# Kernel tuning notes

Measured on AMD Instinct MI355X. Metric: run time of the kernel, lower is better.

The kernel has to match this reference:

```python
import jax, jax.numpy as jnp
import numpy as np

C = 256   # in_channels
H = 48
W = 48
B = 2     # batch after chunking into 3 frames; input batch = 3*B
F = 3     # frames (torch.chunk(x, 3))
G = 4     # GroupNorm groups
EPS = 1e-6


def setup_inputs() -> dict:
    key = jax.random.key(0)
    ks = jax.random.split(key, 10)
    s = C ** -0.5  # keep q/k magnitudes sane so softmax is not saturated
    return {
        "x":    jax.random.normal(ks[0], (F * B, C, H, W), jnp.float32),
        "gn_w": jnp.ones((C,), jnp.float32),
        "gn_b": jnp.zeros((C,), jnp.float32),
        "wq":   jax.random.normal(ks[1], (C, C), jnp.float32) * s,
        "bq":   jax.random.normal(ks[2], (C,), jnp.float32) * 0.02,
        "wk":   jax.random.normal(ks[3], (C, C), jnp.float32) * s,
        "bk":   jax.random.normal(ks[4], (C,), jnp.float32) * 0.02,
        "wv":   jax.random.normal(ks[5], (C, C), jnp.float32) * s,
        "bv":   jax.random.normal(ks[6], (C,), jnp.float32) * 0.02,
        "wp":   jax.random.normal(ks[7], (C, C), jnp.float32) * s,
        "bp":   jax.random.normal(ks[8], (C,), jnp.float32) * 0.02,
    }


def reference(x, gn_w, gn_b, wq, bq, wk, bk, wv, bv, wp, bp):
    B3, c, h, w = x.shape
    b = B3 // F
    # torch.chunk(x, 3) + stack(dim=2) -> (b, c, f, h, w); chunk index is frame
    hx = jnp.moveaxis(x.reshape(F, b, c, h, w), 0, 2)  # (b, c, f, h, w)

    # GroupNorm(num_groups=4, eps=1e-6, affine)
    hg = hx.reshape(b, G, c // G, F, h, w)
    mu = hg.mean(axis=(2, 3, 4, 5), keepdims=True)
    var = hg.var(axis=(2, 3, 4, 5), keepdims=True)
    hn = ((hg - mu) * jax.lax.rsqrt(var + EPS)).reshape(b, c, F, h, w)
    hn = hn * gn_w[None, :, None, None, None] + gn_b[None, :, None, None, None]

    # 1x1x1 Conv3d == channel matmul over flattened tokens n = (f h w)
    n = F * h * w
    hf = hn.reshape(b, c, n)                                  # (b, c, n)
    q = jnp.einsum('oc,bcn->bon', wq, hf) + bq[None, :, None]
    k = jnp.einsum('oc,bcn->bon', wk, hf) + bk[None, :, None]
    v = jnp.einsum('oc,bcn->bon', wv, hf) + bv[None, :, None]

    # scores[b,n,m] = sum_c q[b,c,n] * k[b,c,m], scaled by c^-0.5, softmax over m
    scores = jnp.einsum('bcn,bcm->bnm', q, k) * (c ** -0.5)
    attn = jax.nn.softmax(scores, axis=-1)                    # (b, n, n)

    # out[b,c,n] = sum_m v[b,c,m] * attn[b,n,m]
    o = jnp.einsum('bcm,bnm->bcn', v, attn)
    o = jnp.einsum('oc,bcn->bon', wp, o) + bp[None, :, None]  # proj_out

    o = o.reshape(b, c, F, h, w)
    # permute(0,2,1,3,4) then merge (b f) -> batch (b-major, f-minor)
    o = jnp.moveaxis(o, 2, 1).reshape(B3, c, h, w)
    return x + o
```

## Files before the change

kernel.cpp:

```cpp
#include <hip/hip_runtime.h>
#include <stdint.h>

#define CDIM 256
#define HW 2304
#define FR 3
#define NBATCH 2
#define NTOK 6912
#define EPSV 1e-6f
#define QSCALE (0.0625f * 1.44269504088896f)

typedef __attribute__((ext_vector_type(8))) short short8;
typedef __attribute__((ext_vector_type(4))) short short4v;
typedef __attribute__((ext_vector_type(4))) float f32x4;
typedef __attribute__((ext_vector_type(16))) float f32x16;
typedef __attribute__((ext_vector_type(4))) uint32_t u32x4;
typedef unsigned short u16;

__device__ inline u16 f2bf(float f) {
  union { float f; uint32_t u; } v; v.f = f;
  uint32_t r = v.u + 0x7FFFu + ((v.u >> 16) & 1u);
  return (u16)(r >> 16);
}
__device__ inline float bf2f(u16 h) {
  union { uint32_t u; float f; } v; v.u = ((uint32_t)h) << 16; return v.f;
}
__device__ inline void gload16(const void* g, void* l) {
  __builtin_amdgcn_global_load_lds(
      (const __attribute__((address_space(1))) void*)g,
      (__attribute__((address_space(3))) void*)l, 16, 0, 0);
}

__global__ void pre_k(const float* x, float* part, const float* wq,
                      const float* wk, const float* wv, const float* wp,
                      u16* wb) {
  if (blockIdx.x >= 256) {
    int idx = (blockIdx.x - 256) * 256 + threadIdx.x;
    wb[0 * 65536 + idx] = f2bf(wq[idx] * QSCALE);
    wb[1 * 65536 + idx] = f2bf(wk[idx]);
    wb[2 * 65536 + idx] = f2bf(wv[idx]);
    wb[3 * 65536 + idx] = f2bf(wp[idx]);
    return;
  }
  int bg = blockIdx.x >> 5, sl = blockIdx.x & 31;
  int b = bg >> 2, g = bg & 3;
  int tid = threadIdx.x;
  float s1 = 0.f, s2 = 0.f;
  for (int i = tid; i < 2 * NTOK; i += 256) {
    int cl = sl * 2 + (i / NTOK); int rem = i % NTOK;
    int f = rem / HW; int hw = rem - f * HW;
    float v = x[((size_t)(f * NBATCH + b) * CDIM + g * 64 + cl) * HW + hw];
    s1 += v; s2 += v * v;
  }
  #pragma unroll
  for (int m = 32; m >= 1; m >>= 1) {
    s1 += __shfl_xor(s1, m, 64);
    s2 += __shfl_xor(s2, m, 64);
  }
  __shared__ float r1[4], r2[4];
  int wid = tid >> 6;
  if ((tid & 63) == 0) { r1[wid] = s1; r2[wid] = s2; }
  __syncthreads();
  if (tid == 0) {
    part[blockIdx.x * 2 + 0] = r1[0] + r1[1] + r1[2] + r1[3];
    part[blockIdx.x * 2 + 1] = r2[0] + r2[1] + r2[2] + r2[3];
  }
}

__global__ void gn_fin_k(const float* part, float* stats) {
  int tid = threadIdx.x;
  if (tid < 8) {
    float s1 = 0.f, s2 = 0.f;
    for (int s = 0; s < 32; ++s) {
      s1 += part[(tid * 32 + s) * 2 + 0];
      s2 += part[(tid * 32 + s) * 2 + 1];
    }
    float inv = 1.f / (64.f * NTOK);
    float mu = s1 * inv;
    float var = s2 * inv - mu * mu;
    stats[tid * 2 + 0] = mu;
    stats[tid * 2 + 1] = rsqrtf(var + EPSV);
  }
}

__global__ void gn_apply_k(const float* x, const float* gn_w, const float* gn_b,
                           const float* stats, u16* hn) {
  int nt = blockIdx.x, ct = blockIdx.y, b = blockIdx.z;
  int tid = threadIdx.x;
  __shared__ float tile[64][65];
  int n0 = nt * 64; int f = n0 / HW; int hw0 = n0 - f * HW;
  float mu = stats[(b * 4 + ct) * 2 + 0];
  float rs = stats[(b * 4 + ct) * 2 + 1];
  #pragma unroll
  for (int i = 0; i < 16; ++i) {
    int lin = i * 256 + tid;
    int cr = lin >> 6, nc = lin & 63;
    int c = ct * 64 + cr;
    float v = x[((size_t)(f * NBATCH + b) * CDIM + c) * HW + hw0 + nc];
    tile[cr][nc] = (v - mu) * rs * gn_w[c] + gn_b[c];
  }
  __syncthreads();
  #pragma unroll
  for (int i = 0; i < 16; ++i) {
    int lin = i * 256 + tid;
    int nr = lin >> 6, cc = lin & 63;
    hn[((size_t)b * NTOK + n0 + nr) * CDIM + ct * 64 + cc] = f2bf(tile[cc][nr]);
  }
}

__global__ __launch_bounds__(256) void qkv_k(const u16* hn, const u16* wb,
    const float* bq, const float* bk, const float* bv,
    u16* qb, u16* kb, u16* vb) {
  int nt = blockIdx.x;
  int op = blockIdx.y >> 1, b = blockIdx.y & 1;
  int tid = threadIdx.x, lane = tid & 63, wid = tid >> 6;
  int lr = lane & 15, lg = lane >> 4;
  __shared__ __align__(16) char hn_lds[32768];
  {
    const char* src = (const char*)(hn + ((size_t)b * NTOK + nt * 64) * CDIM);
    #pragma unroll
    for (int i = 0; i < 8; ++i) {
      int off = i * 4096 + wid * 1024 + lane * 16;
      int row = off >> 9;
      gload16(src + (off ^ ((row & 7) << 4)), hn_lds + i * 4096 + wid * 1024);
    }
  }
  __syncthreads();
  f32x4 acc[16];
  #pragma unroll
  for (int i = 0; i < 16; ++i) acc[i] = (f32x4){0.f, 0.f, 0.f, 0.f};
  const u16* wsrc = wb + op * 65536;
  __builtin_amdgcn_s_setprio(1);
  #pragma unroll
  for (int cc = 0; cc < 4; ++cc) {
    short8 afr[2];
    #pragma unroll
    for (int kc = 0; kc < 2; ++kc) {
      int row = wid * 16 + lr;
      int byte = row * 512 + (cc * 64 + kc * 32 + lg * 8) * 2;
      afr[kc] = *(const short8*)(hn_lds + (byte ^ ((row & 7) << 4)));
    }
    #pragma unroll
    for (int cot = 0; cot < 16; ++cot) {
      #pragma unroll
      for (int kc = 0; kc < 2; ++kc) {
        short8 bfr = *(const short8*)(wsrc + (size_t)(cot * 16 + lr) * CDIM +
                                      cc * 64 + kc * 32 + lg * 8);
        if (op == 2)
          acc[cot] = __builtin_amdgcn_mfma_f32_16x16x32_bf16(afr[kc], bfr, acc[cot], 0, 0, 0);
        else
          acc[cot] = __builtin_amdgcn_mfma_f32_16x16x32_bf16(bfr, afr[kc], acc[cot], 0, 0, 0);
      }
    }
  }
  __builtin_amdgcn_s_setprio(0);
  if (op == 2) {
    int m0 = wid * 16 + lg * 4;
    char* vtile = (char*)vb + (size_t)b * NTOK * CDIM * 2 + (size_t)nt * 32768;
    int mchunk = (m0 >> 3);
    #pragma unroll
    for (int cot = 0; cot < 16; ++cot) {
      int co = cot * 16 + lr;
      float bb = bv[co];
      short4v r;
      #pragma unroll
      for (int j = 0; j < 4; ++j) r[j] = (short)f2bf(acc[cot][j] + bb);
      *(short4v*)(vtile + mchunk * 4096 + co * 16 + (lg & 1) * 8) = r;
    }
  } else {
    int row = wid * 16 + lr;
    int n = nt * 64 + row;
    const float* bias = (op == 0) ? bq : bk;
    float bscale = (op == 0) ? QSCALE : 1.0f;
    char* ktile = (char*)kb + (size_t)b * NTOK * CDIM * 2 + (size_t)nt * 32768;
    #pragma unroll
    for (int cot = 0; cot < 16; ++cot) {
      int co = cot * 16 + lg * 4;
      f32x4 b4 = *(const f32x4*)(bias + co);
      short4v r;
      #pragma unroll
      for (int j = 0; j < 4; ++j) r[j] = (short)f2bf(acc[cot][j] + b4[j] * bscale);
      if (op == 0) {
        *(short4v*)(qb + ((size_t)b * NTOK + n) * CDIM + co) = r;
      } else {
        int colchunk = cot * 2 + (lg >> 1);
        *(short4v*)(ktile + colchunk * 1024 + row * 16 + (lg & 1) * 8) = r;
      }
    }
  }
}

template <bool SPLIT>
__global__ __launch_bounds__(512, 2) void flash_k(const u16* qb, const u16* kb,
                                                  const u16* vb, u16* opart,
                                                  float* ml, u16* ob) {
  int qt = blockIdx.x, b = blockIdx.y, sp = blockIdx.z;
  int tid = threadIdx.x, lane = tid & 63, wid = tid >> 6;
  int ln = lane & 31, hi = lane >> 5;
  __shared__ __align__(16) char k_lds[2][32768];
  __shared__ __align__(16) char v_lds[2][32768];

  int t0 = SPLIT ? 27 * sp : 0;
  int t1 = SPLIT ? 27 * sp + 27 : 108;

  int nq = qt * 256 + wid * 32 + ln;
  const u16* qsrc = qb + ((size_t)b * NTOK + nq) * CDIM;
  short8 qf[16];
  #pragma unroll
  for (int ks = 0; ks < 16; ++ks)
    qf[ks] = *(const short8*)(qsrc + ks * 16 + hi * 8);

  float mrun = -1e30f, lrun = 0.f;
  f32x16 o[8];
  #pragma unroll
  for (int i = 0; i < 8; ++i)
    #pragma unroll
    for (int j = 0; j < 16; ++j) o[i][j] = 0.f;

  const char* kbb = (const char*)(kb + (size_t)b * NTOK * CDIM);
  const char* vbb = (const char*)(vb + (size_t)b * NTOK * CDIM);
  int kbase = hi * 1024 + ln * 16;
  int vbase = hi * 4096 + ln * 16;

  {
    const char* ks_ = kbb + (size_t)t0 * 32768;
    const char* vs_ = vbb + (size_t)t0 * 32768;
    #pragma unroll
    for (int i = 0; i < 8; ++i) {
      int ch = i * 8 + wid;
      if (ch < 32) gload16(ks_ + ch * 1024 + lane * 16, k_lds[0] + ch * 1024);
      else gload16(vs_ + (ch - 32) * 1024 + lane * 16, v_lds[0] + (ch - 32) * 1024);
    }
  }
  __syncthreads();

  for (int t = t0; t < t1; ++t) {
    int cur = (t - t0) & 1;
    if (t + 1 < t1) {
      const char* ks_ = kbb + (size_t)(t + 1) * 32768;
      const char* vs_ = vbb + (size_t)(t + 1) * 32768;
      #pragma unroll
      for (int i = 0; i < 8; ++i) {
        int ch = i * 8 + wid;
        if (ch < 32) gload16(ks_ + ch * 1024 + lane * 16, k_lds[cur ^ 1] + ch * 1024);
        else gload16(vs_ + (ch - 32) * 1024 + lane * 16, v_lds[cur ^ 1] + (ch - 32) * 1024);
      }
    }
    const char* kc = k_lds[cur] + kbase;
    const char* vc = v_lds[cur] + vbase;

    #pragma unroll
    for (int mt = 0; mt < 2; ++mt) {
      f32x16 S;
      #pragma unroll
      for (int j = 0; j < 16; ++j) S[j] = 0.f;
      __builtin_amdgcn_s_setprio(1);
      #pragma unroll
      for (int ks = 0; ks < 16; ++ks) {
        short8 kf = *(const short8*)(kc + ks * 2048 + mt * 512);
        S = __builtin_amdgcn_mfma_f32_32x32x16_bf16(kf, qf[ks], S, 0, 0, 0);
      }
      __builtin_amdgcn_s_setprio(0);
      float px = S[0];
      #pragma unroll
      for (int j = 1; j < 16; ++j) px = fmaxf(px, S[j]);
      px = fmaxf(px, __shfl_xor(px, 32, 64));
      if (__any(px > mrun + 10.0f)) {
        float mn = fmaxf(mrun, px);
        float r = exp2f(mrun - mn);
        mrun = mn; lrun *= r;
        #pragma unroll
        for (int i = 0; i < 8; ++i)
          #pragma unroll
          for (int j = 0; j < 16; ++j) o[i][j] *= r;
      }
      float lsum = 0.f;
      #pragma unroll
      for (int j = 0; j < 16; ++j) {
        float p = exp2f(S[j] - mrun);
        S[j] = p; lsum += p;
      }
      lsum += __shfl_xor(lsum, 32, 64);
      lrun += lsum;
      #pragma unroll
      for (int lks = 0; lks < 2; ++lks) {
        int rb = lks * 8;
        uint32_t x0, x1, y0, y1;
        asm("v_cvt_pk_bf16_f32 %0, %1, %2" : "=v"(x0) : "v"(S[rb + 0]), "v"(S[rb + 1]));
        asm("v_cvt_pk_bf16_f32 %0, %1, %2" : "=v"(x1) : "v"(S[rb + 2]), "v"(S[rb + 3]));
        asm("v_cvt_pk_bf16_f32 %0, %1, %2" : "=v"(y0) : "v"(S[rb + 4]), "v"(S[rb + 5]));
        asm("v_cvt_pk_bf16_f32 %0, %1, %2" : "=v"(y1) : "v"(S[rb + 6]), "v"(S[rb + 7]));
        asm("v_permlane32_swap_b32 %0, %1" : "+v"(x0), "+v"(y0));
        asm("v_permlane32_swap_b32 %0, %1" : "+v"(x1), "+v"(y1));
        u32x4 pd = (u32x4){x0, x1, y0, y1};
        short8 pf = *(short8*)&pd;
        __builtin_amdgcn_s_setprio(1);
        #pragma unroll
        for (int ct = 0; ct < 8; ++ct) {
          short8 vf = *(const short8*)(vc + (mt * 2 + lks) * 8192 + ct * 512);
          o[ct] = __builtin_amdgcn_mfma_f32_32x32x16_bf16(vf, pf, o[ct], 0, 0, 0);
        }
        __builtin_amdgcn_s_setprio(0);
      }
    }
    __syncthreads();
  }

  if (!SPLIT) {
    float linv = 1.0f / lrun;
    u16* d0 = ob + ((size_t)b * NTOK + nq) * CDIM;
    #pragma unroll
    for (int ct = 0; ct < 8; ++ct) {
      #pragma unroll
      for (int rq = 0; rq < 4; ++rq) {
        short4v r4;
        #pragma unroll
        for (int j = 0; j < 4; ++j) r4[j] = (short)f2bf(o[ct][rq * 4 + j] * linv);
        *(short4v*)(d0 + ct * 32 + rq * 8 + hi * 4) = r4;
      }
    }
  } else {
    u16* d0 = opart + ((size_t)(sp * 2 + b) * NTOK + nq) * CDIM;
    #pragma unroll
    for (int ct = 0; ct < 8; ++ct) {
      #pragma unroll
      for (int rq = 0; rq < 4; ++rq) {
        short4v r4;
        #pragma unroll
        for (int j = 0; j < 4; ++j) r4[j] = (short)f2bf(o[ct][rq * 4 + j]);
        *(short4v*)(d0 + ct * 32 + rq * 8 + hi * 4) = r4;
      }
    }
    if (hi == 0) {
      size_t mb = (size_t)(sp * 2 + b) * 2;
      ml[(mb + 0) * NTOK + nq] = mrun;
      ml[(mb + 1) * NTOK + nq] = lrun;
    }
  }
}

template <bool SPLIT>
__global__ __launch_bounds__(256) void proj_k(const u16* ob, const u16* opart,
    const float* ml, const u16* wb, const float* bp, const float* x, float* out) {
  int nt = blockIdx.x, b = blockIdx.y;
  int tid = threadIdx.x, lane = tid & 63, wid = tid >> 6;
  int lr = lane & 15, lg = lane >> 4;
  __shared__ __align__(16) char o_lds[32768];
  const u16* wpb = wb + 3 * 65536;
  if (SPLIT) {
    #pragma unroll
    for (int i = 0; i < 8; ++i) {
      int off = i * 4096 + tid * 16;
      int row = off >> 9;
      int c0 = (off & 511) >> 1;
      int n = nt * 64 + row;
      float mm[4], llv[4];
      #pragma unroll
      for (int s = 0; s < 4; ++s) {
        mm[s] = ml[((size_t)(s * 2 + b) * 2 + 0) * NTOK + n];
        llv[s] = ml[((size_t)(s * 2 + b) * 2 + 1) * NTOK + n];
      }
      float M = fmaxf(fmaxf(mm[0], mm[1]), fmaxf(mm[2], mm[3]));
      float w[4]; float den = 0.f;
      #pragma unroll
      for (int s = 0; s < 4; ++s) { w[s] = exp2f(mm[s] - M); den += w[s] * llv[s]; }
      float inv = 1.f / den;
      float o[8] = {0.f, 0.f, 0.f, 0.f, 0.f, 0.f, 0.f, 0.f};
      #pragma unroll
      for (int s = 0; s < 4; ++s) {
        short8 v = *(const short8*)(opart + ((size_t)(s * 2 + b) * NTOK + n) * CDIM + c0);
        #pragma unroll
        for (int j = 0; j < 8; ++j) o[j] += w[s] * bf2f((u16)v[j]);
      }
      short8 r8;
      #pragma unroll
      for (int j = 0; j < 8; ++j) r8[j] = (short)f2bf(o[j] * inv);
      *(short8*)(o_lds + (off ^ ((row & 7) << 4))) = r8;
    }
  } else {
    const char* src = (const char*)(ob + ((size_t)b * NTOK + nt * 64) * CDIM);
    #pragma unroll
    for (int i = 0; i < 8; ++i) {
      int off = i * 4096 + wid * 1024 + lane * 16;
      int row = off >> 9;
      gload16(src + (off ^ ((row & 7) << 4)), o_lds + i * 4096 + wid * 1024);
    }
  }
  __syncthreads();
  #pragma unroll
  for (int ct2 = 0; ct2 < 4; ++ct2) {
    int cot = wid * 4 + ct2;
    short8 aw[8];
    #pragma unroll
    for (int kc = 0; kc < 8; ++kc)
      aw[kc] = *(const short8*)(wpb + (size_t)(cot * 16 + lr) * CDIM + kc * 32 + lg * 8);
    #pragma unroll
    for (int ntile = 0; ntile < 4; ++ntile) {
      f32x4 a = (f32x4){0.f, 0.f, 0.f, 0.f};
      #pragma unroll
      for (int kc = 0; kc < 8; ++kc) {
        int row = ntile * 16 + lr;
        int byte = row * 512 + (kc * 32 + lg * 8) * 2;
        short8 bfr = *(const short8*)(o_lds + (byte ^ ((row & 7) << 4)));
        a = __builtin_amdgcn_mfma_f32_16x16x32_bf16(aw[kc], bfr, a, 0, 0, 0);
      }
      int n = nt * 64 + ntile * 16 + lr;
      int f = n / HW; int hw = n - f * HW;
      #pragma unroll
      for (int j = 0; j < 4; ++j) {
        int co = cot * 16 + lg * 4 + j;
        float val = a[j] + bp[co];
        size_t oi = ((size_t)(b * FR + f) * CDIM + co) * HW + hw;
        out[oi] = x[oi] + val;
      }
    }
  }
}

extern "C" void kernel_launch(void* const* d_in, const int* in_sizes, int n_in,
                              void* d_out, int out_size, void* d_ws, size_t ws_size,
                              hipStream_t stream) {
  const float* x    = (const float*)d_in[0];
  const float* gn_w = (const float*)d_in[1];
  const float* gn_b = (const float*)d_in[2];
  const float* wq   = (const float*)d_in[3];
  const float* bq   = (const float*)d_in[4];
  const float* wk   = (const float*)d_in[5];
  const float* bk   = (const float*)d_in[6];
  const float* wv   = (const float*)d_in[7];
  const float* bv   = (const float*)d_in[8];
  const float* wp   = (const float*)d_in[9];
  const float* bp   = (const float*)d_in[10];
  float* out = (float*)d_out;
  char* ws = (char*)d_ws;

  float* stats = (float*)(ws + 0);
  float* part  = (float*)(ws + 256);
  u16* wb = (u16*)(ws + 4096);
  u16* hn = (u16*)(ws + 528384);
  u16* qb = (u16*)(ws + 7606272);
  u16* kb = (u16*)(ws + 14684160);
  u16* vb = (u16*)(ws + 21762048);
  u16* ob = (u16*)(ws + 28839936);
  u16* opart = (u16*)(ws + 35917824);
  float* ml  = (float*)(ws + 64229376);
  const size_t NEED_SPLIT = 64671744;

  pre_k<<<512, 256, 0, stream>>>(x, part, wq, wk, wv, wp, wb);
  gn_fin_k<<<1, 64, 0, stream>>>(part, stats);
  gn_apply_k<<<dim3(108, 4, 2), 256, 0, stream>>>(x, gn_w, gn_b, stats, hn);
  qkv_k<<<dim3(108, 6), 256, 0, stream>>>(hn, wb, bq, bk, bv, qb, kb, vb);
  if (ws_size >= NEED_SPLIT) {
    flash_k<true><<<dim3(27, 2, 4), 512, 0, stream>>>(qb, kb, vb, opart, ml, ob);
    proj_k<true><<<dim3(108, 2), 256, 0, stream>>>(ob, opart, ml, wb, bp, x, out);
  } else {
    flash_k<false><<<dim3(27, 2, 1), 512, 0, stream>>>(qb, kb, vb, opart, ml, ob);
    proj_k<false><<<dim3(108, 2), 256, 0, stream>>>(ob, opart, ml, wb, bp, x, out);
  }
}
```

Before: 216.3 us.

## Fuse GroupNorm finalize, apply and QKV projection into one kernel

Merges the GroupNorm stats finalization, normalization/transpose and QKV projection into a single kernel. Each block now reduces the partial sums itself, normalizes its 64-token tile straight into LDS as bf16, and loops over the three projections. This removes two kernel launches and the global round trip of the normalized activation buffer. In exchange the grid shrinks from 648 to 216 blocks, each doing three times the matmul work, which lowers parallelism on a many-CU device.

```diff
diff --git a/kernel.cpp b/kernel.cpp
--- a/kernel.cpp
+++ b/kernel.cpp
@@ -66,124 +66,125 @@
   }
 }
 
-__global__ void gn_fin_k(const float* part, float* stats) {
-  int tid = threadIdx.x;
-  if (tid < 8) {
-    float s1 = 0.f, s2 = 0.f;
-    for (int s = 0; s < 32; ++s) {
-      s1 += part[(tid * 32 + s) * 2 + 0];
-      s2 += part[(tid * 32 + s) * 2 + 1];
-    }
-    float inv = 1.f / (64.f * NTOK);
-    float mu = s1 * inv;
-    float var = s2 * inv - mu * mu;
-    stats[tid * 2 + 0] = mu;
-    stats[tid * 2 + 1] = rsqrtf(var + EPSV);
-  }
-}
-
-__global__ void gn_apply_k(const float* x, const float* gn_w, const float* gn_b,
-                           const float* stats, u16* hn) {
-  int nt = blockIdx.x, ct = blockIdx.y, b = blockIdx.z;
-  int tid = threadIdx.x;
-  __shared__ float tile[64][65];
-  int n0 = nt * 64; int f = n0 / HW; int hw0 = n0 - f * HW;
-  float mu = stats[(b * 4 + ct) * 2 + 0];
-  float rs = stats[(b * 4 + ct) * 2 + 1];
-  #pragma unroll
-  for (int i = 0; i < 16; ++i) {
-    int lin = i * 256 + tid;
-    int cr = lin >> 6, nc = lin & 63;
-    int c = ct * 64 + cr;
-    float v = x[((size_t)(f * NBATCH + b) * CDIM + c) * HW + hw0 + nc];
-    tile[cr][nc] = (v - mu) * rs * gn_w[c] + gn_b[c];
-  }
-  __syncthreads();
-  #pragma unroll
-  for (int i = 0; i < 16; ++i) {
-    int lin = i * 256 + tid;
-    int nr = lin >> 6, cc = lin & 63;
-    hn[((size_t)b * NTOK + n0 + nr) * CDIM + ct * 64 + cc] = f2bf(tile[cc][nr]);
-  }
-}
-
-__global__ __launch_bounds__(256) void qkv_k(const u16* hn, const u16* wb,
+__global__ __launch_bounds__(256) void qkvf_k(const float* x, const float* part,
+    const float* gn_w, const float* gn_b, const u16* wb,
     const float* bq, const float* bk, const float* bv,
     u16* qb, u16* kb, u16* vb) {
-  int nt = blockIdx.x;
-  int op = blockIdx.y >> 1, b = blockIdx.y & 1;
+  int nt = blockIdx.x, b = blockIdx.y;
   int tid = threadIdx.x, lane = tid & 63, wid = tid >> 6;
   int lr = lane & 15, lg = lane >> 4;
   __shared__ __align__(16) char hn_lds[32768];
-  {
-    const char* src = (const char*)(hn + ((size_t)b * NTOK + nt * 64) * CDIM);
+  __shared__ float tile[64][65];
+  __shared__ float sstat[8];
+
+  if (tid < 128) {
+    int g = (tid >> 5) & 3, s = tid & 31;
+    float p1 = part[((b * 4 + g) * 32 + s) * 2 + 0];
+    float p2 = part[((b * 4 + g) * 32 + s) * 2 + 1];
+    #pragma unroll
+    for (int m = 1; m < 32; m <<= 1) {
+      p1 += __shfl_xor(p1, m, 64);
+      p2 += __shfl_xor(p2, m, 64);
+    }
+    if (s == 0) {
+      float inv = 1.f / (64.f * NTOK);
+      float mu = p1 * inv;
+      float var = p2 * inv - mu * mu;
+      sstat[g * 2 + 0] = mu;
+      sstat[g * 2 + 1] = rsqrtf(var + EPSV);
+    }
+  }
+  __syncthreads();
+
+  int n0 = nt * 64; int f = n0 / HW; int hw0 = n0 - f * HW;
+  #pragma unroll
+  for (int ct = 0; ct < 4; ++ct) {
+    float mu = sstat[ct * 2 + 0];
+    float rs = sstat[ct * 2 + 1];
+    #pragma unroll
+    for (int i = 0; i < 16; ++i) {
+      int lin = i * 256 + tid;
+      int cr = lin >> 6, nc = lin & 63;
+      int c = ct * 64 + cr;
+      float v = x[((size_t)(f * NBATCH + b) * CDIM + c) * HW + hw0 + nc];
+      tile[cr][nc] = (v - mu) * rs * gn_w[c] + gn_b[c];
+    }
+    __syncthreads();
     #pragma unroll
     for (int i = 0; i < 8; ++i) {
-      int off = i * 4096 + wid * 1024 + lane * 16;
-      int row = off >> 9;
-      gload16(src + (off ^ ((row & 7) << 4)), hn_lds + i * 4096 + wid * 1024);
-    }
-  }
-  __syncthreads();
-  f32x4 acc[16];
-  #pragma unroll
-  for (int i = 0; i < 16; ++i) acc[i] = (f32x4){0.f, 0.f, 0.f, 0.f};
-  const u16* wsrc = wb + op * 65536;
-  __builtin_amdgcn_s_setprio(1);
-  #pragma unroll
-  for (int cc = 0; cc < 4; ++cc) {
-    short8 afr[2];
-    #pragma unroll
-    for (int kc = 0; kc < 2; ++kc) {
+      int lin = i * 256 + tid;
+      int nr = lin >> 5, cp = lin & 31;
+      int cc = cp * 2;
+      uint32_t pk = (uint32_t)f2bf(tile[cc][nr]) |
+                    ((uint32_t)f2bf(tile[cc + 1][nr]) << 16);
+      int byte = nr * 512 + (ct * 64 + cc) * 2;
+      *(uint32_t*)(hn_lds + (byte ^ ((nr & 7) << 4))) = pk;
+    }
+    __syncthreads();
+  }
+
+  #pragma unroll
+  for (int op = 0; op < 3; ++op) {
+    f32x4 acc[16];
+    #pragma unroll
+    for (int i = 0; i < 16; ++i) acc[i] = (f32x4){0.f, 0.f, 0.f, 0.f};
+    const u16* wsrc = wb + op * 65536;
+    __builtin_amdgcn_s_setprio(1);
+    #pragma unroll
+    for (int cc = 0; cc < 4; ++cc) {
+      short8 afr[2];
+      #pragma unroll
+      for (int kc = 0; kc < 2; ++kc) {
+        int row = wid * 16 + lr;
+        int byte = row * 512 + (cc * 64 + kc * 32 + lg * 8) * 2;
+        afr[kc] = *(const short8*)(hn_lds + (byte ^ ((row & 7) << 4)));
+      }
+      #pragma unroll
+      for (int cot = 0; cot < 16; ++cot) {
+        #pragma unroll
+        for (int kc = 0; kc < 2; ++kc) {
+          short8 bfr = *(const short8*)(wsrc + (size_t)(cot * 16 + lr) * CDIM +
+                                        cc * 64 + kc * 32 + lg * 8);
+          if (op == 2)
+            acc[cot] = __builtin_amdgcn_mfma_f32_16x16x32_bf16(afr[kc], bfr, acc[cot], 0, 0, 0);
+          else
+            acc[cot] = __builtin_amdgcn_mfma_f32_16x16x32_bf16(bfr, afr[kc], acc[cot], 0, 0, 0);
+        }
+      }
+    }
+    __builtin_amdgcn_s_setprio(0);
+    if (op == 2) {
+      int m0 = wid * 16 + lg * 4;
+      char* vtile = (char*)vb + (size_t)b * NTOK * CDIM * 2 + (size_t)nt * 32768;
+      int mchunk = (m0 >> 3);
+      #pragma unroll
+      for (int cot = 0; cot < 16; ++cot) {
+        int co = cot * 16 + lr;
+        float bb = bv[co];
+        short4v r;
+        #pragma unroll
+        for (int j = 0; j < 4; ++j) r[j] = (short)f2bf(acc[cot][j] + bb);
+        *(short4v*)(vtile + mchunk * 4096 + co * 16 + (lg & 1) * 8) = r;
+      }
+    } else {
       int row = wid * 16 + lr;
-      int byte = row * 512 + (cc * 64 + kc * 32 + lg * 8) * 2;
-      afr[kc] = *(const short8*)(hn_lds + (byte ^ ((row & 7) << 4)));
-    }
-    #pragma unroll
-    for (int cot = 0; cot < 16; ++cot) {
-      #pragma unroll
-      for (int kc = 0; kc < 2; ++kc) {
-        short8 bfr = *(const short8*)(wsrc + (size_t)(cot * 16 + lr) * CDIM +
-                                      cc * 64 + kc * 32 + lg * 8);
-        if (op == 2)
-          acc[cot] = __builtin_amdgcn_mfma_f32_16x16x32_bf16(afr[kc], bfr, acc[cot], 0, 0, 0);
-        else
-          acc[cot] = __builtin_amdgcn_mfma_f32_16x16x32_bf16(bfr, afr[kc], acc[cot], 0, 0, 0);
-      }
-    }
-  }
-  __builtin_amdgcn_s_setprio(0);
-  if (op == 2) {
-    int m0 = wid * 16 + lg * 4;
-    char* vtile = (char*)vb + (size_t)b * NTOK * CDIM * 2 + (size_t)nt * 32768;
-    int mchunk = (m0 >> 3);
-    #pragma unroll
-    for (int cot = 0; cot < 16; ++cot) {
-      int co = cot * 16 + lr;
-      float bb = bv[co];
-      short4v r;
-      #pragma unroll
-      for (int j = 0; j < 4; ++j) r[j] = (short)f2bf(acc[cot][j] + bb);
-      *(short4v*)(vtile + mchunk * 4096 + co * 16 + (lg & 1) * 8) = r;
-    }
-  } else {
-    int row = wid * 16 + lr;
-    int n = nt * 64 + row;
-    const float* bias = (op == 0) ? bq : bk;
-    float bscale = (op == 0) ? QSCALE : 1.0f;
-    char* ktile = (char*)kb + (size_t)b * NTOK * CDIM * 2 + (size_t)nt * 32768;
-    #pragma unroll
-    for (int cot = 0; cot < 16; ++cot) {
-      int co = cot * 16 + lg * 4;
-      f32x4 b4 = *(const f32x4*)(bias + co);
-      short4v r;
-      #pragma unroll
-      for (int j = 0; j < 4; ++j) r[j] = (short)f2bf(acc[cot][j] + b4[j] * bscale);
-      if (op == 0) {
-        *(short4v*)(qb + ((size_t)b * NTOK + n) * CDIM + co) = r;
-      } else {
-        int colchunk = cot * 2 + (lg >> 1);
-        *(short4v*)(ktile + colchunk * 1024 + row * 16 + (lg & 1) * 8) = r;
+      int n = nt * 64 + row;
+      const float* bias = (op == 0) ? bq : bk;
+      float bscale = (op == 0) ? QSCALE : 1.0f;
+      char* ktile = (char*)kb + (size_t)b * NTOK * CDIM * 2 + (size_t)nt * 32768;
+      #pragma unroll
+      for (int cot = 0; cot < 16; ++cot) {
+        int co = cot * 16 + lg * 4;
+        f32x4 b4 = *(const f32x4*)(bias + co);
+        short4v r;
+        #pragma unroll
+        for (int j = 0; j < 4; ++j) r[j] = (short)f2bf(acc[cot][j] + b4[j] * bscale);
+        if (op == 0) {
+          *(short4v*)(qb + ((size_t)b * NTOK + n) * CDIM + co) = r;
+        } else {
+          int colchunk = cot * 2 + (lg >> 1);
+          *(short4v*)(ktile + colchunk * 1024 + row * 16 + (lg & 1) * 8) = r;
+        }
       }
     }
   }
@@ -433,10 +434,8 @@
   float* out = (float*)d_out;
   char* ws = (char*)d_ws;
 
-  float* stats = (float*)(ws + 0);
   float* part  = (float*)(ws + 256);
   u16* wb = (u16*)(ws + 4096);
-  u16* hn = (u16*)(ws + 528384);
   u16* qb = (u16*)(ws + 7606272);
   u16* kb = (u16*)(ws + 14684160);
   u16* vb = (u16*)(ws + 21762048);
@@ -446,9 +445,8 @@
   const size_t NEED_SPLIT = 64671744;
 
   pre_k<<<512, 256, 0, stream>>>(x, part, wq, wk, wv, wp, wb);
-  gn_fin_k<<<1, 64, 0, stream>>>(part, stats);
-  gn_apply_k<<<dim3(108, 4, 2), 256, 0, stream>>>(x, gn_w, gn_b, stats, hn);
-  qkv_k<<<dim3(108, 6), 256, 0, stream>>>(hn, wb, bq, bk, bv, qb, kb, vb);
+  qkvf_k<<<dim3(108, 2), 256, 0, stream>>>(x, part, gn_w, gn_b, wb,
+                                           bq, bk, bv, qb, kb, vb);
   if (ws_size >= NEED_SPLIT) {
     flash_k<true><<<dim3(27, 2, 4), 512, 0, stream>>>(qb, kb, vb, opart, ml, ob);
     proj_k<true><<<dim3(108, 2), 256, 0, stream>>>(ob, opart, ml, wb, bp, x, out);
```

After: 255.7 us. +18.2%, slower.
